# Optimization experiments

Hardware: AMD Instinct MI355X
Metric: run time of the kernel (lower is better)

Reference implementation:

```python
import jax, jax.numpy as jnp
import numpy as np

NUM_EMBEDDINGS = 4096
EMBEDDING_DIM = 128
COMMITMENT_COST = 0.25


def setup_inputs() -> dict:
    key = jax.random.key(0)
    k_x, k_w = jax.random.split(key)
    inputs = jax.random.normal(k_x, (32, 128, 32, 32), dtype=jnp.float32)
    # xavier_uniform for Embedding weight [K, D]: bound = sqrt(6/(K+D))
    bound = float(np.sqrt(6.0 / (NUM_EMBEDDINGS + EMBEDDING_DIM)))
    weight = jax.random.uniform(k_w, (NUM_EMBEDDINGS, EMBEDDING_DIM),
                                dtype=jnp.float32, minval=-bound, maxval=bound)
    return {"inputs": inputs, "weight": weight}


def reference(inputs, weight):
    K, D = weight.shape
    # channels-first 4D input with C == embedding_dim -> NHWC
    x = jnp.transpose(inputs, (0, 2, 3, 1))  # [B, H, W, D]
    input_shape = x.shape
    flat = x.reshape(-1, D)                  # [N, D]

    x_sq = jnp.sum(flat * flat, axis=1, keepdims=True)          # [N, 1]
    w_sq = jnp.sum(weight * weight, axis=1)                     # [K]
    two_xy = 2.0 * jnp.matmul(flat, weight.T)                   # [N, K]
    distances = x_sq - two_xy + w_sq[None, :] + 1e-8

    encoding_indices = jnp.argmin(distances, axis=1)            # [N] int

    quantized = weight[encoding_indices].reshape(input_shape)   # [B, H, W, D]

    q_latent_loss = jnp.mean((quantized - x) ** 2)
    e_latent_loss = jnp.mean((jax.lax.stop_gradient(quantized) - x) ** 2)
    loss = q_latent_loss + COMMITMENT_COST * e_latent_loss
    loss = jnp.where(jnp.isnan(loss) | jnp.isinf(loss), jnp.float32(0.1), loss)

    quantized_st = x + jax.lax.stop_gradient(quantized - x)

    counts = jnp.zeros((K,), dtype=jnp.float32).at[encoding_indices].add(1.0)
    avg_probs = counts / encoding_indices.shape[0]
    perplexity = jnp.exp(-jnp.sum(avg_probs * jnp.log(avg_probs + 1e-10)))

    encodings = jax.nn.one_hot(encoding_indices, K, dtype=jnp.float32)  # [N, K]

    # input was channels-first -> restore NCHW
    quantized_st = jnp.transpose(quantized_st, (0, 3, 1, 2))
    return quantized_st, loss, perplexity, encodings, encoding_indices
```

## Files before the change

### kernel.cpp

```cpp
#include <hip/hip_runtime.h>
#include <stdint.h>
#include <math.h>

#define K_CODES 4096
#define DIM 128
#define N_FLAT 32768
#define HW 1024

#define OFF_Q    0
#define OFF_LOSS 4194304
#define OFF_PERP 4194305
#define OFF_ENC  4194306
#define OFF_IDX  138412034

#define WS_PACKED 0
#define WS_COUNTS 262144
#define WS_WSQ    278528
#define WS_XSQ    294912
#define WS_PART   425984
#define WS_XHL    430080
#define WS_WHL    (WS_XHL + 16777216)

typedef _Float16 f16x8 __attribute__((ext_vector_type(8)));
typedef float    f32x4 __attribute__((ext_vector_type(4)));


__global__ __launch_bounds__(256) void wsq_kernel(const float* __restrict__ w,
                                                  float* __restrict__ wsq,
                                                  float* __restrict__ counts) {
    int wave = threadIdx.x >> 6, lane = threadIdx.x & 63;
    int k = blockIdx.x * 4 + wave;
    float a = w[k * DIM + lane];
    float b = w[k * DIM + lane + 64];
    float s = a * a + b * b;
    #pragma unroll
    for (int o = 32; o > 0; o >>= 1) s += __shfl_down(s, o, 64);
    if (lane == 0) { wsq[k] = s; counts[k] = 0.f; }
}

__global__ __launch_bounds__(256) void wplanes_kernel(const float* __restrict__ w,
                                                      _Float16* __restrict__ whl) {
    int T = blockIdx.x * 256 + threadIdx.x;
    int k = T >> 2, seg = T & 3;
    const float* wp = w + (size_t)k * DIM + seg * 32;
    _Float16* row = whl + (size_t)k * 256;
    #pragma unroll
    for (int q = 0; q < 4; ++q) {
        float4 a = *(const float4*)(wp + q * 8);
        float4 b = *(const float4*)(wp + q * 8 + 4);
        float vv[8] = {a.x, a.y, a.z, a.w, b.x, b.y, b.z, b.w};
        f16x8 hv, lv;
        #pragma unroll
        for (int j = 0; j < 8; ++j) {
            float v = 1024.0f * vv[j];
            _Float16 h = (_Float16)v;
            _Float16 l = (_Float16)(v - (float)h);
            hv[j] = h; lv[j] = l;
        }
        *(f16x8*)(row + seg * 32 + q * 8) = hv;
        *(f16x8*)(row + 128 + seg * 32 + q * 8) = lv;
    }
}

__global__ __launch_bounds__(256) void xprep_kernel(const float* __restrict__ x,
                                                    _Float16* __restrict__ xhl,
                                                    float* __restrict__ xsq,
                                                    unsigned long long* __restrict__ packed) {
    __shared__ float xt[128 * 65];
    const int t = threadIdx.x;
    const int n0 = blockIdx.x * 64;
    const int b = n0 >> 10, hw0 = n0 & 1023;
    const float* xg = x + (size_t)b * (DIM * HW) + hw0;
    #pragma unroll
    for (int i = 0; i < 16; ++i) {
        int idx = i * 256 + t;
        int c = idx >> 5, n2 = (idx & 31) << 1;
        float2 v = *(const float2*)(xg + c * HW + n2);
        xt[c * 65 + n2] = v.x;
        xt[c * 65 + n2 + 1] = v.y;
    }
    __syncthreads();
    if (t < 64) {
        packed[n0 + t] = ~0ull;
        float s = 0.f;
        #pragma unroll
        for (int c = 0; c < DIM; ++c) {
            float v = xt[c * 65 + t];
            s = fmaf(v, v, s);
        }
        xsq[n0 + t] = s;
    }
    const int n = t >> 2, seg = t & 3;
    _Float16* row = xhl + (size_t)(n0 + n) * 256;
    #pragma unroll
    for (int q = 0; q < 4; ++q) {
        f16x8 hv, lv;
        #pragma unroll
        for (int j = 0; j < 8; ++j) {
            float v = 32.0f * xt[(seg * 32 + q * 8 + j) * 65 + n];
            _Float16 h = (_Float16)v;
            _Float16 l = (_Float16)(v - (float)h);
            hv[j] = h; lv[j] = l;
        }
        *(f16x8*)(row + seg * 32 + q * 8) = hv;
        *(f16x8*)(row + 128 + seg * 32 + q * 8) = lv;
    }
}

__global__ __launch_bounds__(256) void dist_argmin(
    const _Float16* __restrict__ xhl, const _Float16* __restrict__ whl,
    const float* __restrict__ wsq, const float* __restrict__ xsq,
    unsigned long long* __restrict__ packed, float* __restrict__ enc)
{
    __shared__ __align__(16) _Float16 xl[128 * 72];
    __shared__ __align__(16) _Float16 wl[128 * 72];
    __shared__ float xsq_s[128], wsq_s[128];
    __shared__ unsigned long long red[128][2];

    const int tid  = threadIdx.x;
    const int lane = tid & 63, wave = tid >> 6;
    const int lq   = lane & 15, quad = lane >> 4;
    const int wn0  = (wave >> 1) * 64, wk0 = (wave & 1) * 64;
    const int n0   = blockIdx.x * 128;
    const int kbase = blockIdx.y * 512;

    const int sr = tid >> 3, sh = (tid >> 2) & 1, sq = tid & 3;

    {
        float* ebase = enc + (size_t)n0 * K_CODES + kbase;
        float4 z4; z4.x = z4.y = z4.z = z4.w = 0.f;
        #pragma unroll 8
        for (int i = 0; i < 64; ++i) {
            int idx = i * 256 + tid;
            int r = idx >> 7, c4 = idx & 127;
            *(float4*)(ebase + (size_t)r * K_CODES + 2 + c4 * 4) = z4;
        }
        if (tid < 128) {
            float2 z2; z2.x = 0.f; z2.y = 0.f;
            *(float2*)(ebase + (size_t)tid * K_CODES) = z2;
        }
    }

    if (tid < 128) xsq_s[tid] = xsq[n0 + tid];

    const _Float16* xbase = xhl + (size_t)n0 * 256;

    for (int ks = 0; ks < 4; ++ks) {
        const int k0 = kbase + ks * 128;
        if (tid < 128) wsq_s[tid] = wsq[k0 + tid];
        const _Float16* wbase = whl + (size_t)k0 * 256;

        f32x4 acc[4][4];
        #pragma unroll
        for (int i = 0; i < 4; ++i)
            #pragma unroll
            for (int j = 0; j < 4; ++j)
                acc[i][j] = (f32x4){0.f, 0.f, 0.f, 0.f};

        #pragma unroll
        for (int c0 = 0; c0 < 4; ++c0) {
            __syncthreads();
            #pragma unroll
            for (int i = 0; i < 4; ++i) {
                int r = sr + i * 32;
                int goff = r * 256 + sh * 128 + c0 * 32 + sq * 8;
                int loff = r * 72 + sh * 32 + sq * 8;
                *(f16x8*)(xl + loff) = *(const f16x8*)(xbase + goff);
                *(f16x8*)(wl + loff) = *(const f16x8*)(wbase + goff);
            }
            __syncthreads();

            f16x8 ah[4], al[4], bh[4], bl[4];
            #pragma unroll
            for (int i = 0; i < 4; ++i) {
                int xrow = (wn0 + i * 16 + lq) * 72 + quad * 8;
                ah[i] = *(const f16x8*)(xl + xrow);
                al[i] = *(const f16x8*)(xl + xrow + 32);
                int wrow = (wk0 + i * 16 + lq) * 72 + quad * 8;
                bh[i] = *(const f16x8*)(wl + wrow);
                bl[i] = *(const f16x8*)(wl + wrow + 32);
            }
            #pragma unroll
            for (int ki = 0; ki < 4; ++ki)
                #pragma unroll
                for (int ni = 0; ni < 4; ++ni) {
                    acc[ni][ki] = __builtin_amdgcn_mfma_f32_16x16x32_f16(
                        ah[ni], bh[ki], acc[ni][ki], 0, 0, 0);
                    acc[ni][ki] = __builtin_amdgcn_mfma_f32_16x16x32_f16(
                        ah[ni], bl[ki], acc[ni][ki], 0, 0, 0);
                    acc[ni][ki] = __builtin_amdgcn_mfma_f32_16x16x32_f16(
                        al[ni], bh[ki], acc[ni][ki], 0, 0, 0);
                }
        }

        #pragma unroll
        for (int ni = 0; ni < 4; ++ni) {
            #pragma unroll
            for (int rg = 0; rg < 4; ++rg) {
                int rowl = wn0 + ni * 16 + quad * 4 + rg;
                float xr = xsq_s[rowl];
                float best = 3.4e38f; int bk = 0;
                #pragma unroll
                for (int ki = 0; ki < 4; ++ki) {
                    int kl = wk0 + ki * 16 + lq;
                    float t = xr - acc[ni][ki][rg] * 6.103515625e-05f;
                    t += wsq_s[kl];
                    t += 1e-8f;
                    if (t < best) { best = t; bk = k0 + kl; }
                }
                unsigned u = __float_as_uint(best);
                u = (u & 0x80000000u) ? ~u : (u | 0x80000000u);
                unsigned long long p =
                    ((unsigned long long)u << 32) | (unsigned)bk;
                #pragma unroll
                for (int m = 1; m < 16; m <<= 1) {
                    unsigned long long o = __shfl_xor(p, m, 64);
                    if (o < p) p = o;
                }
                if (lq == 0) red[rowl][wave & 1] = p;
            }
        }
        __syncthreads();
        if (tid < 128) {
            unsigned long long a = red[tid][0], b = red[tid][1];
            atomicMin(&packed[n0 + tid], a < b ? a : b);
        }
    }
}

__global__ __launch_bounds__(256) void combine(
    const unsigned long long* __restrict__ packed,
    float* __restrict__ idxf, float* __restrict__ enc,
    float* __restrict__ counts)
{
    int n = blockIdx.x * 256 + threadIdx.x;
    unsigned k = (unsigned)(packed[n] & 0xFFFFFFFFu);
    idxf[n] = (float)k;
    enc[(size_t)n * K_CODES + k] = 1.0f;
    atomicAdd(&counts[k], 1.0f);
}

__global__ __launch_bounds__(256) void quantize_loss(
    const float* __restrict__ x, const float* __restrict__ w,
    const float* __restrict__ idxf, float* __restrict__ outq,
    float* __restrict__ part)
{
    const int base4 = (blockIdx.x * 256 + threadIdx.x) * 4;
    float s = 0.f;
    #pragma unroll
    for (int i = 0; i < 4; ++i) {
        int e  = base4 + i * 1048576;
        int hw = e & 1023;
        int c  = (e >> 10) & 127;
        int b  = e >> 17;
        int n  = (b << 10) | hw;
        float4 xv = *(const float4*)(x + e);
        float4 kf = *(const float4*)(idxf + n);
        float q0 = w[(int)kf.x * DIM + c];
        float q1 = w[(int)kf.y * DIM + c];
        float q2 = w[(int)kf.z * DIM + c];
        float q3 = w[(int)kf.w * DIM + c];
        float4 df; df.x = q0 - xv.x; df.y = q1 - xv.y;
                   df.z = q2 - xv.z; df.w = q3 - xv.w;
        float4 o;  o.x = xv.x + df.x; o.y = xv.y + df.y;
                   o.z = xv.z + df.z; o.w = xv.w + df.w;
        *(float4*)(outq + e) = o;
        s = fmaf(df.x, df.x, s);
        s = fmaf(df.y, df.y, s);
        s = fmaf(df.z, df.z, s);
        s = fmaf(df.w, df.w, s);
    }
    #pragma unroll
    for (int o = 32; o > 0; o >>= 1) s += __shfl_down(s, o, 64);
    __shared__ float ls[4];
    if ((threadIdx.x & 63) == 0) ls[threadIdx.x >> 6] = s;
    __syncthreads();
    if (threadIdx.x == 0) part[blockIdx.x] = ls[0] + ls[1] + ls[2] + ls[3];
}

__global__ __launch_bounds__(256) void finalize(
    const float* __restrict__ counts, const float* __restrict__ part,
    float* __restrict__ out)
{
    __shared__ float sh[512];
    float h = 0.f;
    for (int k = threadIdx.x; k < K_CODES; k += 256) {
        float p = counts[k] * (1.0f / N_FLAT);
        h += p * logf(p + 1e-10f);
    }
    float s = 0.f;
    for (int i = threadIdx.x; i < 1024; i += 256) s += part[i];
    sh[threadIdx.x] = h;
    sh[256 + threadIdx.x] = s;
    __syncthreads();
    #pragma unroll
    for (int st = 128; st > 0; st >>= 1) {
        if (threadIdx.x < st) {
            sh[threadIdx.x] += sh[threadIdx.x + st];
            sh[256 + threadIdx.x] += sh[256 + threadIdx.x + st];
        }
        __syncthreads();
    }
    if (threadIdx.x == 0) {
        float perp = expf(-sh[0]);
        float loss = 1.25f * (sh[256] / 4194304.0f);
        if (isnan(loss) || isinf(loss)) loss = 0.1f;
        out[OFF_LOSS] = loss;
        out[OFF_PERP] = perp;
    }
}

extern "C" void kernel_launch(void* const* d_in, const int* in_sizes, int n_in,
                              void* d_out, int out_size, void* d_ws, size_t ws_size,
                              hipStream_t stream) {
    const float* x = (const float*)d_in[0];
    const float* w = (const float*)d_in[1];
    float* out = (float*)d_out;
    char* ws = (char*)d_ws;

    unsigned long long* packed = (unsigned long long*)(ws + WS_PACKED);
    float* counts = (float*)(ws + WS_COUNTS);
    float* wsq    = (float*)(ws + WS_WSQ);
    float* xsq    = (float*)(ws + WS_XSQ);
    float* part   = (float*)(ws + WS_PART);
    _Float16* xhl = (_Float16*)(ws + WS_XHL);
    _Float16* whl = (_Float16*)(ws + WS_WHL);

    wsq_kernel<<<K_CODES / 4, 256, 0, stream>>>(w, wsq, counts);
    wplanes_kernel<<<K_CODES * 4 / 256, 256, 0, stream>>>(w, whl);
    xprep_kernel<<<N_FLAT / 64, 256, 0, stream>>>(x, xhl, xsq, packed);

    dim3 g2(256, 8);
    dist_argmin<<<g2, 256, 0, stream>>>(xhl, whl, wsq, xsq, packed,
                                        out + OFF_ENC);

    combine<<<N_FLAT / 256, 256, 0, stream>>>(packed, out + OFF_IDX,
                                              out + OFF_ENC, counts);

    quantize_loss<<<1024, 256, 0, stream>>>(x, w, out + OFF_IDX,
                                            out + OFF_Q, part);

    finalize<<<1, 256, 0, stream>>>(counts, part, out);
}
```

Before: 846.7 us.

## Register-prefetch next tile, keep running argmin in registers, load wsq directly

Global loads for the next K-chunk of x and codebook tiles are issued into registers before the current chunk's MFMA work, so memory latency overlaps compute. Per-row best distance and index are now kept in registers across all four codebook sub-tiles, and the shuffle reduction plus atomicMin happen once at the end instead of four times. wsq values are read straight into registers, removing the shared array and its stores. The cost is more live registers (prefetch buffers and 32 best values), which may reduce occupancy.

Result: slower. 875.5 us (+3.4%).

```diff
diff --git a/kernel.cpp b/kernel.cpp
--- a/kernel.cpp
+++ b/kernel.cpp
@@ -114,7 +114,7 @@
 {
     __shared__ __align__(16) _Float16 xl[128 * 72];
     __shared__ __align__(16) _Float16 wl[128 * 72];
-    __shared__ float xsq_s[128], wsq_s[128];
+    __shared__ float xsq_s[128];
     __shared__ unsigned long long red[128][2];
 
     const int tid  = threadIdx.x;
@@ -125,6 +125,21 @@
     const int kbase = blockIdx.y * 512;
 
     const int sr = tid >> 3, sh = (tid >> 2) & 1, sq = tid & 3;
+    const int gsub = sh * 128 + sq * 8;
+    const int lsub = sh * 32 + sq * 8;
+
+    const _Float16* xbase = xhl + (size_t)n0 * 256;
+    const _Float16* wbase0 = whl + (size_t)kbase * 256;
+
+    f16x8 px[4], pw[4];
+    #pragma unroll
+    for (int i = 0; i < 4; ++i) {
+        int r = sr + i * 32;
+        px[i] = *(const f16x8*)(xbase + r * 256 + gsub);
+        pw[i] = *(const f16x8*)(wbase0 + r * 256 + gsub);
+    }
+
+    if (tid < 128) xsq_s[tid] = xsq[n0 + tid];
 
     {
         float* ebase = enc + (size_t)n0 * K_CODES + kbase;
@@ -141,14 +156,19 @@
         }
     }
 
-    if (tid < 128) xsq_s[tid] = xsq[n0 + tid];
-
-    const _Float16* xbase = xhl + (size_t)n0 * 256;
+    float bestf[4][4];
+    int   bestk[4][4];
+    #pragma unroll
+    for (int i = 0; i < 4; ++i)
+        #pragma unroll
+        for (int j = 0; j < 4; ++j) { bestf[i][j] = 3.4e38f; bestk[i][j] = 0; }
 
     for (int ks = 0; ks < 4; ++ks) {
         const int k0 = kbase + ks * 128;
-        if (tid < 128) wsq_s[tid] = wsq[k0 + tid];
-        const _Float16* wbase = whl + (size_t)k0 * 256;
+        float wsq_r[4];
+        #pragma unroll
+        for (int ki = 0; ki < 4; ++ki)
+            wsq_r[ki] = wsq[k0 + wk0 + ki * 16 + lq];
 
         f32x4 acc[4][4];
         #pragma unroll
@@ -162,11 +182,20 @@
             __syncthreads();
             #pragma unroll
             for (int i = 0; i < 4; ++i) {
-                int r = sr + i * 32;
-                int goff = r * 256 + sh * 128 + c0 * 32 + sq * 8;
-                int loff = r * 72 + sh * 32 + sq * 8;
-                *(f16x8*)(xl + loff) = *(const f16x8*)(xbase + goff);
-                *(f16x8*)(wl + loff) = *(const f16x8*)(wbase + goff);
+                int loff = (sr + i * 32) * 72 + lsub;
+                *(f16x8*)(xl + loff) = px[i];
+                *(f16x8*)(wl + loff) = pw[i];
+            }
+            const int t = ks * 4 + c0;
+            if (t < 15) {
+                const int tn = t + 1, ksn = tn >> 2, c0n = tn & 3;
+                const _Float16* wbn = whl + (size_t)(kbase + ksn * 128) * 256;
+                #pragma unroll
+                for (int i = 0; i < 4; ++i) {
+                    int r = sr + i * 32;
+                    px[i] = *(const f16x8*)(xbase + r * 256 + c0n * 32 + gsub);
+                    pw[i] = *(const f16x8*)(wbn + r * 256 + c0n * 32 + gsub);
+                }
             }
             __syncthreads();
 
@@ -199,32 +228,41 @@
             for (int rg = 0; rg < 4; ++rg) {
                 int rowl = wn0 + ni * 16 + quad * 4 + rg;
                 float xr = xsq_s[rowl];
-                float best = 3.4e38f; int bk = 0;
                 #pragma unroll
                 for (int ki = 0; ki < 4; ++ki) {
-                    int kl = wk0 + ki * 16 + lq;
                     float t = xr - acc[ni][ki][rg] * 6.103515625e-05f;
-                    t += wsq_s[kl];
+                    t += wsq_r[ki];
                     t += 1e-8f;
-                    if (t < best) { best = t; bk = k0 + kl; }
+                    if (t < bestf[ni][rg]) {
+                        bestf[ni][rg] = t;
+                        bestk[ni][rg] = k0 + wk0 + ki * 16 + lq;
+                    }
                 }
-                unsigned u = __float_as_uint(best);
-                u = (u & 0x80000000u) ? ~u : (u | 0x80000000u);
-                unsigned long long p =
-                    ((unsigned long long)u << 32) | (unsigned)bk;
-                #pragma unroll
-                for (int m = 1; m < 16; m <<= 1) {
-                    unsigned long long o = __shfl_xor(p, m, 64);
-                    if (o < p) p = o;
-                }
-                if (lq == 0) red[rowl][wave & 1] = p;
-            }
-        }
-        __syncthreads();
-        if (tid < 128) {
-            unsigned long long a = red[tid][0], b = red[tid][1];
-            atomicMin(&packed[n0 + tid], a < b ? a : b);
-        }
+            }
+        }
+    }
+
+    #pragma unroll
+    for (int ni = 0; ni < 4; ++ni) {
+        #pragma unroll
+        for (int rg = 0; rg < 4; ++rg) {
+            int rowl = wn0 + ni * 16 + quad * 4 + rg;
+            unsigned u = __float_as_uint(bestf[ni][rg]);
+            u = (u & 0x80000000u) ? ~u : (u | 0x80000000u);
+            unsigned long long p =
+                ((unsigned long long)u << 32) | (unsigned)bestk[ni][rg];
+            #pragma unroll
+            for (int m = 1; m < 16; m <<= 1) {
+                unsigned long long o = __shfl_xor(p, m, 64);
+                if (o < p) p = o;
+            }
+            if (lq == 0) red[rowl][wave & 1] = p;
+        }
+    }
+    __syncthreads();
+    if (tid < 128) {
+        unsigned long long a = red[tid][0], b = red[tid][1];
+        atomicMin(&packed[n0 + tid], a < b ? a : b);
     }
 }
 
```
